# Performance work log

Hardware: AMD Instinct MI355X
Metric: run time of the kernel (lower is better)

## Reference

```python
import jax, jax.numpy as jnp
import numpy as np

B_SZ, SEQ, H, P, N, LBLK = 16, 2048, 16, 64, 16, 64  # batch, seqlen, heads, d_head, d_state, block_len


def setup_inputs() -> dict:
    key = jax.random.key(0)
    k1, k2, k3, k4 = jax.random.split(key, 4)
    X = jax.random.normal(k1, (B_SZ, SEQ, H, P), jnp.float32)
    # A is a per-step log-decay; real Mamba2 has A < 0 so exp(segsum) stays bounded
    A = -0.1 * jax.random.uniform(k2, (B_SZ, SEQ, H), jnp.float32)
    B = jax.random.normal(k3, (B_SZ, SEQ, H, N), jnp.float32)
    C = jax.random.normal(k4, (B_SZ, SEQ, H, N), jnp.float32)
    return {"X": X, "A": A, "B": B, "C": C}


def _exp_segsum(x):
    """x: (..., t). Returns exp(cumsum[i]-cumsum[j]) for j<=i, 0 above diagonal."""
    t = x.shape[-1]
    cs = jnp.cumsum(x, axis=-1)
    diff = cs[..., :, None] - cs[..., None, :]
    mask = jnp.tril(jnp.ones((t, t), dtype=bool))
    return jnp.where(mask, jnp.exp(jnp.where(mask, diff, 0.0)), 0.0)


def ssd_forward(X, A, B, C):
    b, s, h, p = X.shape
    n = B.shape[-1]
    c = s // LBLK
    # chunk: (b, c, l, h, *)
    Xb = X.reshape(b, c, LBLK, h, p)
    Bb = B.reshape(b, c, LBLK, h, n)
    Cb = C.reshape(b, c, LBLK, h, n)
    Ab = jnp.transpose(A.reshape(b, c, LBLK, h), (0, 3, 1, 2))  # (b, h, c, l)
    A_cs = jnp.cumsum(Ab, axis=-1)                               # (b, h, c, l)

    # 1. intra-chunk (diagonal block) output: kernel 1
    L = _exp_segsum(Ab)                                          # (b, h, c, l, s)
    CB = jnp.einsum("bclhn,bcshn->bhcls", Cb, Bb)               # (b, h, c, l, s)
    Y_diag = jnp.einsum("bhcls,bcshp->bclhp", CB * L, Xb)

    # 2. per-chunk end states: kernel 2
    decay_states = jnp.exp(A_cs[..., -1:] - A_cs)                # (b, h, c, l)
    states = jnp.einsum("bclhn,bhcl,bclhp->bchpn", Bb, decay_states, Xb)

    # 3. inter-chunk recurrence (zero initial state): kernel 3
    states = jnp.concatenate([jnp.zeros_like(states[:, :1]), states], axis=1)  # (b, c+1, h, p, n)
    A_last_pad = jnp.pad(A_cs[..., -1], ((0, 0), (0, 0), (1, 0)))              # (b, h, c+1)
    decay_chunk = _exp_segsum(A_last_pad)                                       # (b, h, c+1, c+1)
    new_states = jnp.einsum("bhzc,bchpn->bzhpn", decay_chunk, states)
    states_in = new_states[:, :-1]                                              # (b, c, h, p, n)

    # 4. off-diagonal (state -> output) contribution: kernel 4
    Y_off = jnp.einsum("bclhn,bchpn,bhcl->bclhp", Cb, states_in, jnp.exp(A_cs))

    return (Y_diag + Y_off).reshape(b, s, h, p)


def reference(X, A, B, C):
    return ssd_forward(X, A, B, C)
```

## Files before the change

kernel.cpp:

```cpp
#include <hip/hip_runtime.h>

#define BS 16
#define SEQL 2048
#define NH 16
#define PD 64
#define ND 16
#define LB 64
#define NC 32
#define NHP (NH * PD)
#define NHN (NH * ND)

typedef __attribute__((ext_vector_type(8))) short bf16x8;
typedef __attribute__((ext_vector_type(4))) float f32x4;

static __device__ __forceinline__ unsigned short f2bf(float x) {
  unsigned int u = __float_as_uint(x);
  return (unsigned short)((u + 0x7FFFu + ((u >> 16) & 1u)) >> 16);
}
static __device__ __forceinline__ unsigned int pk2(float a, float b) {
  return (unsigned int)f2bf(a) | ((unsigned int)f2bf(b) << 16);
}

static __device__ __forceinline__ void barrier_lds() {
  __builtin_amdgcn_sched_barrier(0);
  asm volatile("s_waitcnt lgkmcnt(0)" ::: "memory");
  __builtin_amdgcn_s_barrier();
  __builtin_amdgcn_sched_barrier(0);
}

__global__ __launch_bounds__(512, 2) void ssd_fused(
    const float* __restrict__ Xg, const float* __restrict__ Ag,
    const float* __restrict__ Bg, const float* __restrict__ Cg,
    float* __restrict__ Yg) {
  const int h = blockIdx.x & (NH - 1);
  const int b = blockIdx.x >> 4;
  const int t = threadIdx.x;
  const int w = t >> 6;
  const int lane = t & 63;
  const int g = lane >> 4;
  const int cc = lane & 15;

  __shared__ __align__(16) unsigned short sXt[PD][LB + 8];
  __shared__ __align__(16) unsigned short sM [LB][LB + 8];
  __shared__ __align__(16) unsigned short sB [LB][ND + 8];
  __shared__ __align__(16) unsigned short sC [LB][ND + 8];
  __shared__ __align__(16) unsigned short sBdT[ND][LB + 8];
  __shared__ __align__(16) float          sSTf[2][PD][ND + 4];
  __shared__ __align__(16) unsigned short sSTb[2][PD][ND + 8];

  for (int i = t; i < PD * (ND + 4); i += 512) ((float*)sSTf[0])[i] = 0.f;
  for (int i = t; i < PD * (ND + 8); i += 512) ((unsigned short*)sSTb[0])[i] = 0;

  const int xl0 = (t >> 4) * 2, xp0 = (t & 15) * 4;
  const int bl  = t >> 3,       bn0 = (t & 7) * 2;
  float4 px0, px1; float2 pb2, pc2; float pa;

#define PREF(cc_) do { \
    const size_t s0_ = (size_t)(b * SEQL + (cc_) * LB); \
    px0 = *(const float4*)&Xg[(s0_ + xl0) * NHP + h * PD + xp0]; \
    px1 = *(const float4*)&Xg[(s0_ + xl0 + 1) * NHP + h * PD + xp0]; \
    pb2 = *(const float2*)&Bg[(s0_ + bl) * NHN + h * ND + bn0]; \
    pc2 = *(const float2*)&Cg[(s0_ + bl) * NHN + h * ND + bn0]; \
    pa  = Ag[(s0_ + lane) * NH + h]; \
  } while (0)

  PREF(0);

  for (int c = 0; c < NC; ++c) {
    float v = pa;
#pragma unroll
    for (int d = 1; d < 64; d <<= 1) {
      float o = __shfl_up(v, d, 64);
      if (lane >= d) v += o;
    }
    const float acs = v;
    const float er = expf(acs);
    const float rr = expf(-acs);
    const float etot = __shfl(er, 63);

    {
#pragma unroll
      for (int j = 0; j < 4; ++j) {
        const float xa = (&px0.x)[j], xb = (&px1.x)[j];
        *(unsigned int*)&sXt[xp0 + j][xl0] = pk2(xa, xb);
      }
      const float el = __shfl(er, bl);
      const float dl = etot * __shfl(rr, bl);
      *(unsigned int*)&sB[bl][bn0] = pk2(pb2.x, pb2.y);
      *(unsigned int*)&sC[bl][bn0] = pk2(el * pc2.x, el * pc2.y);
      sBdT[bn0][bl]     = f2bf(dl * pb2.x);
      sBdT[bn0 + 1][bl] = f2bf(dl * pb2.y);
    }
    if (c + 1 < NC) PREF(c + 1);
    barrier_lds();

    {
      const int lb1 = w & 3;
      const int l = lb1 * 16 + cc;
      bf16x8 zf = {0, 0, 0, 0, 0, 0, 0, 0};
      bf16x8 cf = zf;
      if (g < 2) cf = *(const bf16x8*)&sC[l][g * 8];
#pragma unroll
      for (int ii = 0; ii < 2; ++ii) {
        const int sb = (w < 4 ? 0 : 2) + ii;
        uint2 out = make_uint2(0u, 0u);
        if (sb <= lb1) {
          bf16x8 bfr = zf;
          if (g < 2) bfr = *(const bf16x8*)&sB[sb * 16 + cc][g * 8];
          f32x4 z4 = {0.f, 0.f, 0.f, 0.f};
          f32x4 d = __builtin_amdgcn_mfma_f32_16x16x32_bf16(bfr, cf, z4, 0, 0, 0);
          float m[4];
#pragma unroll
          for (int r = 0; r < 4; ++r) {
            const int srow = sb * 16 + 4 * g + r;
            m[r] = d[r] * __shfl(rr, srow);
            if (sb == lb1 && (4 * g + r) > cc) m[r] = 0.f;
          }
          out.x = pk2(m[0], m[1]);
          out.y = pk2(m[2], m[3]);
        }
        *(uint2*)&sM[l][sb * 16 + g * 4] = out;
      }
    }
    barrier_lds();

    const int cur = c & 1, nxt = cur ^ 1;
    if (w < 4) {
      const int lb = w;
      const int l = lb * 16 + cc;
      bf16x8 zf = {0, 0, 0, 0, 0, 0, 0, 0};
      bf16x8 cf = zf;
      if (g < 2) cf = *(const bf16x8*)&sC[l][g * 8];
      bf16x8 a0 = *(const bf16x8*)&sM[l][g * 8];
      bf16x8 a1 = zf;
      if (lb >= 2) a1 = *(const bf16x8*)&sM[l][32 + g * 8];
#pragma unroll
      for (int pb = 0; pb < 4; ++pb) {
        const int p = pb * 16 + cc;
        bf16x8 stf = zf;
        if (g < 2) stf = *(const bf16x8*)&sSTb[cur][p][g * 8];
        f32x4 acc = {0.f, 0.f, 0.f, 0.f};
        acc = __builtin_amdgcn_mfma_f32_16x16x32_bf16(cf, stf, acc, 0, 0, 0);
        bf16x8 xf0 = *(const bf16x8*)&sXt[p][g * 8];
        acc = __builtin_amdgcn_mfma_f32_16x16x32_bf16(a0, xf0, acc, 0, 0, 0);
        if (lb >= 2) {
          bf16x8 xf1 = *(const bf16x8*)&sXt[p][32 + g * 8];
          acc = __builtin_amdgcn_mfma_f32_16x16x32_bf16(a1, xf1, acc, 0, 0, 0);
        }
        const size_t yb =
            ((size_t)(b * SEQL + c * LB + lb * 16 + 4 * g)) * NHP + h * PD + p;
#pragma unroll
        for (int r = 0; r < 4; ++r)
          Yg[yb + (size_t)r * NHP] = acc[r];
      }
    } else {
      const int pb = w - 4;
      const int p = pb * 16 + cc;
      bf16x8 ad0 = *(const bf16x8*)&sBdT[cc][g * 8];
      bf16x8 ad1 = *(const bf16x8*)&sBdT[cc][32 + g * 8];
      bf16x8 xt0 = *(const bf16x8*)&sXt[p][g * 8];
      bf16x8 xt1 = *(const bf16x8*)&sXt[p][32 + g * 8];
      f32x4 acc = {0.f, 0.f, 0.f, 0.f};
      acc = __builtin_amdgcn_mfma_f32_16x16x32_bf16(ad0, xt0, acc, 0, 0, 0);
      acc = __builtin_amdgcn_mfma_f32_16x16x32_bf16(ad1, xt1, acc, 0, 0, 0);
      float4 old = *(const float4*)&sSTf[cur][p][4 * g];
      float4 nw;
      nw.x = old.x * etot + acc[0];
      nw.y = old.y * etot + acc[1];
      nw.z = old.z * etot + acc[2];
      nw.w = old.w * etot + acc[3];
      *(float4*)&sSTf[nxt][p][4 * g] = nw;
      uint2 ub;
      ub.x = pk2(nw.x, nw.y);
      ub.y = pk2(nw.z, nw.w);
      *(uint2*)&sSTb[nxt][p][4 * g] = ub;
    }
    barrier_lds();
  }
#undef PREF
}

extern "C" void kernel_launch(void* const* d_in, const int* in_sizes, int n_in,
                              void* d_out, int out_size, void* d_ws, size_t ws_size,
                              hipStream_t stream) {
  (void)in_sizes; (void)n_in; (void)out_size; (void)d_ws; (void)ws_size;
  const float* X = (const float*)d_in[0];
  const float* A = (const float*)d_in[1];
  const float* B = (const float*)d_in[2];
  const float* C = (const float*)d_in[3];
  float* Y = (float*)d_out;
  ssd_fused<<<BS * NH, 512, 0, stream>>>(X, A, B, C, Y);
}
```

Before: 80.15 us.

## Keep decay matrix in registers, precompute cumsums, swizzle X tile in LDS

Precomputes all chunk cumsums and exponentials for A once into shared memory at kernel start, removing the per-chunk shuffle scan. Drops the sM LDS round-trip and one barrier per chunk by having each Y-wave compute its masked CB*L tiles directly into MFMA operand registers. It also XOR-swizzles the transposed X tile with a K-permutation so fragments load with fewer bank conflicts, and removes the occupancy hint from launch bounds. In exchange the Y waves take on the extra MFMA and scaling work, and the state waves sit idle during that phase.

```diff
diff --git a/kernel.cpp b/kernel.cpp
--- a/kernel.cpp
+++ b/kernel.cpp
@@ -28,7 +28,13 @@
   __builtin_amdgcn_sched_barrier(0);
 }
 
-__global__ __launch_bounds__(512, 2) void ssd_fused(
+static __device__ __forceinline__ int invperm(int l) {
+  const int jp = l >> 5, v = l & 31;
+  return jp * 32 + (v < 16 ? (((v >> 2) << 3) | (v & 3))
+                           : ((((v - 16) >> 2) << 3) | 4 | ((v - 16) & 3)));
+}
+
+__global__ __launch_bounds__(512) void ssd_fused(
     const float* __restrict__ Xg, const float* __restrict__ Ag,
     const float* __restrict__ Bg, const float* __restrict__ Cg,
     float* __restrict__ Yg) {
@@ -40,140 +46,155 @@
   const int g = lane >> 4;
   const int cc = lane & 15;
 
-  __shared__ __align__(16) unsigned short sXt[PD][LB + 8];
-  __shared__ __align__(16) unsigned short sM [LB][LB + 8];
-  __shared__ __align__(16) unsigned short sB [LB][ND + 8];
-  __shared__ __align__(16) unsigned short sC [LB][ND + 8];
+  __shared__ __align__(16) unsigned short sXt[PD][64];
+  __shared__ __align__(16) unsigned short sB[LB][ND + 8];
+  __shared__ __align__(16) unsigned short sC[LB][ND + 8];
   __shared__ __align__(16) unsigned short sBdT[ND][LB + 8];
-  __shared__ __align__(16) float          sSTf[2][PD][ND + 4];
+  __shared__ __align__(16) float sSTf[2][PD][ND + 4];
   __shared__ __align__(16) unsigned short sSTb[2][PD][ND + 8];
-
+  __shared__ float sER[NC][LB];
+  __shared__ float sRR[NC][LB];
+  __shared__ float sEtot[NC];
+
+  {
+    float av[4];
+#pragma unroll
+    for (int k = 0; k < 4; ++k)
+      av[k] = Ag[((size_t)(b * SEQL + (w + 8 * k) * LB + lane)) * NH + h];
+#pragma unroll
+    for (int k = 0; k < 4; ++k) {
+      const int c = w + 8 * k;
+      float v = av[k];
+#pragma unroll
+      for (int d = 1; d < 64; d <<= 1) {
+        float o = __shfl_up(v, d, 64);
+        if (lane >= d) v += o;
+      }
+      const float e = expf(v);
+      sER[c][lane] = e;
+      sRR[c][lane] = expf(-v);
+      if (lane == 63) sEtot[c] = e;
+    }
+  }
   for (int i = t; i < PD * (ND + 4); i += 512) ((float*)sSTf[0])[i] = 0.f;
   for (int i = t; i < PD * (ND + 8); i += 512) ((unsigned short*)sSTb[0])[i] = 0;
 
   const int xl0 = (t >> 4) * 2, xp0 = (t & 15) * 4;
-  const int bl  = t >> 3,       bn0 = (t & 7) * 2;
-  float4 px0, px1; float2 pb2, pc2; float pa;
-
-#define PREF(cc_) do { \
-    const size_t s0_ = (size_t)(b * SEQL + (cc_) * LB); \
+  const int bl = t >> 3, bn0 = (t & 7) * 2;
+  const int mX = invperm(xl0);
+  const int mB = invperm(bl);
+  float4 px0, px1;
+  float2 pb2, pc2;
+
+#define PREF(ci) do { \
+    const size_t s0_ = (size_t)(b * SEQL + (ci) * LB); \
     px0 = *(const float4*)&Xg[(s0_ + xl0) * NHP + h * PD + xp0]; \
     px1 = *(const float4*)&Xg[(s0_ + xl0 + 1) * NHP + h * PD + xp0]; \
     pb2 = *(const float2*)&Bg[(s0_ + bl) * NHN + h * ND + bn0]; \
     pc2 = *(const float2*)&Cg[(s0_ + bl) * NHN + h * ND + bn0]; \
-    pa  = Ag[(s0_ + lane) * NH + h]; \
   } while (0)
 
+  const bf16x8 zf8 = {0, 0, 0, 0, 0, 0, 0, 0};
+  auto xfrag = [&](int p_, int kb) -> bf16x8 {
+    return *(const bf16x8*)&sXt[p_][(kb ^ ((p_ >> 3) & 7)) << 3];
+  };
+
   PREF(0);
+  __syncthreads();
 
   for (int c = 0; c < NC; ++c) {
-    float v = pa;
-#pragma unroll
-    for (int d = 1; d < 64; d <<= 1) {
-      float o = __shfl_up(v, d, 64);
-      if (lane >= d) v += o;
-    }
-    const float acs = v;
-    const float er = expf(acs);
-    const float rr = expf(-acs);
-    const float etot = __shfl(er, 63);
-
     {
 #pragma unroll
       for (int j = 0; j < 4; ++j) {
-        const float xa = (&px0.x)[j], xb = (&px1.x)[j];
-        *(unsigned int*)&sXt[xp0 + j][xl0] = pk2(xa, xb);
-      }
-      const float el = __shfl(er, bl);
-      const float dl = etot * __shfl(rr, bl);
+        const int p_ = xp0 + j;
+        const int mm = ((((mX >> 3) ^ ((p_ >> 3) & 7)) << 3) | (mX & 7));
+        *(unsigned int*)&sXt[p_][mm] = pk2((&px0.x)[j], (&px1.x)[j]);
+      }
+      const float el = sER[c][bl];
+      const float dl = sEtot[c] * sRR[c][bl];
       *(unsigned int*)&sB[bl][bn0] = pk2(pb2.x, pb2.y);
       *(unsigned int*)&sC[bl][bn0] = pk2(el * pc2.x, el * pc2.y);
-      sBdT[bn0][bl]     = f2bf(dl * pb2.x);
-      sBdT[bn0 + 1][bl] = f2bf(dl * pb2.y);
+      sBdT[bn0][mB] = f2bf(dl * pb2.x);
+      sBdT[bn0 + 1][mB] = f2bf(dl * pb2.y);
     }
     if (c + 1 < NC) PREF(c + 1);
-    barrier_lds();
-
-    {
-      const int lb1 = w & 3;
-      const int l = lb1 * 16 + cc;
-      bf16x8 zf = {0, 0, 0, 0, 0, 0, 0, 0};
-      bf16x8 cf = zf;
-      if (g < 2) cf = *(const bf16x8*)&sC[l][g * 8];
-#pragma unroll
-      for (int ii = 0; ii < 2; ++ii) {
-        const int sb = (w < 4 ? 0 : 2) + ii;
-        uint2 out = make_uint2(0u, 0u);
-        if (sb <= lb1) {
-          bf16x8 bfr = zf;
-          if (g < 2) bfr = *(const bf16x8*)&sB[sb * 16 + cc][g * 8];
-          f32x4 z4 = {0.f, 0.f, 0.f, 0.f};
-          f32x4 d = __builtin_amdgcn_mfma_f32_16x16x32_bf16(bfr, cf, z4, 0, 0, 0);
-          float m[4];
-#pragma unroll
-          for (int r = 0; r < 4; ++r) {
-            const int srow = sb * 16 + 4 * g + r;
-            m[r] = d[r] * __shfl(rr, srow);
-            if (sb == lb1 && (4 * g + r) > cc) m[r] = 0.f;
-          }
-          out.x = pk2(m[0], m[1]);
-          out.y = pk2(m[2], m[3]);
-        }
-        *(uint2*)&sM[l][sb * 16 + g * 4] = out;
-      }
-    }
     barrier_lds();
 
     const int cur = c & 1, nxt = cur ^ 1;
     if (w < 4) {
       const int lb = w;
       const int l = lb * 16 + cc;
-      bf16x8 zf = {0, 0, 0, 0, 0, 0, 0, 0};
-      bf16x8 cf = zf;
+      bf16x8 cf = zf8;
       if (g < 2) cf = *(const bf16x8*)&sC[l][g * 8];
-      bf16x8 a0 = *(const bf16x8*)&sM[l][g * 8];
-      bf16x8 a1 = zf;
-      if (lb >= 2) a1 = *(const bf16x8*)&sM[l][32 + g * 8];
+      auto mtile = [&](int sb, bool mask) -> uint2 {
+        bf16x8 bfr = zf8;
+        if (g < 2) bfr = *(const bf16x8*)&sB[sb * 16 + cc][g * 8];
+        f32x4 z4 = {0.f, 0.f, 0.f, 0.f};
+        f32x4 d = __builtin_amdgcn_mfma_f32_16x16x32_bf16(bfr, cf, z4, 0, 0, 0);
+        float m[4];
+#pragma unroll
+        for (int r = 0; r < 4; ++r) {
+          m[r] = d[r] * sRR[c][sb * 16 + 4 * g + r];
+          if (mask && (4 * g + r) > cc) m[r] = 0.f;
+        }
+        return make_uint2(pk2(m[0], m[1]), pk2(m[2], m[3]));
+      };
+      union {
+        bf16x8 v;
+        unsigned int u[4];
+      } mf0, mf1;
+      mf0.u[0] = mf0.u[1] = mf0.u[2] = mf0.u[3] = 0u;
+      mf1.u[0] = mf1.u[1] = mf1.u[2] = mf1.u[3] = 0u;
+      if (lb == 0) {
+        const uint2 t0 = mtile(0, true);
+        mf0.u[0] = t0.x; mf0.u[1] = t0.y;
+      } else if (lb == 1) {
+        const uint2 t0 = mtile(0, false), t1 = mtile(1, true);
+        mf0.u[0] = t0.x; mf0.u[1] = t0.y; mf0.u[2] = t1.x; mf0.u[3] = t1.y;
+      } else if (lb == 2) {
+        const uint2 t0 = mtile(0, false), t1 = mtile(1, false), t2 = mtile(2, true);
+        mf0.u[0] = t0.x; mf0.u[1] = t0.y; mf0.u[2] = t1.x; mf0.u[3] = t1.y;
+        mf1.u[0] = t2.x; mf1.u[1] = t2.y;
+      } else {
+        const uint2 t0 = mtile(0, false), t1 = mtile(1, false);
+        const uint2 t2 = mtile(2, false), t3 = mtile(3, true);
+        mf0.u[0] = t0.x; mf0.u[1] = t0.y; mf0.u[2] = t1.x; mf0.u[3] = t1.y;
+        mf1.u[0] = t2.x; mf1.u[1] = t2.y; mf1.u[2] = t3.x; mf1.u[3] = t3.y;
+      }
 #pragma unroll
       for (int pb = 0; pb < 4; ++pb) {
         const int p = pb * 16 + cc;
-        bf16x8 stf = zf;
+        bf16x8 stf = zf8;
         if (g < 2) stf = *(const bf16x8*)&sSTb[cur][p][g * 8];
         f32x4 acc = {0.f, 0.f, 0.f, 0.f};
         acc = __builtin_amdgcn_mfma_f32_16x16x32_bf16(cf, stf, acc, 0, 0, 0);
-        bf16x8 xf0 = *(const bf16x8*)&sXt[p][g * 8];
-        acc = __builtin_amdgcn_mfma_f32_16x16x32_bf16(a0, xf0, acc, 0, 0, 0);
-        if (lb >= 2) {
-          bf16x8 xf1 = *(const bf16x8*)&sXt[p][32 + g * 8];
-          acc = __builtin_amdgcn_mfma_f32_16x16x32_bf16(a1, xf1, acc, 0, 0, 0);
-        }
+        acc = __builtin_amdgcn_mfma_f32_16x16x32_bf16(mf0.v, xfrag(p, g), acc, 0, 0, 0);
+        if (lb >= 2)
+          acc = __builtin_amdgcn_mfma_f32_16x16x32_bf16(mf1.v, xfrag(p, 4 + g), acc, 0, 0, 0);
         const size_t yb =
             ((size_t)(b * SEQL + c * LB + lb * 16 + 4 * g)) * NHP + h * PD + p;
 #pragma unroll
-        for (int r = 0; r < 4; ++r)
-          Yg[yb + (size_t)r * NHP] = acc[r];
+        for (int r = 0; r < 4; ++r) Yg[yb + (size_t)r * NHP] = acc[r];
       }
     } else {
-      const int pb = w - 4;
-      const int p = pb * 16 + cc;
+      const int pS = (w - 4) * 16 + cc;
       bf16x8 ad0 = *(const bf16x8*)&sBdT[cc][g * 8];
       bf16x8 ad1 = *(const bf16x8*)&sBdT[cc][32 + g * 8];
-      bf16x8 xt0 = *(const bf16x8*)&sXt[p][g * 8];
-      bf16x8 xt1 = *(const bf16x8*)&sXt[p][32 + g * 8];
-      f32x4 acc = {0.f, 0.f, 0.f, 0.f};
-      acc = __builtin_amdgcn_mfma_f32_16x16x32_bf16(ad0, xt0, acc, 0, 0, 0);
-      acc = __builtin_amdgcn_mfma_f32_16x16x32_bf16(ad1, xt1, acc, 0, 0, 0);
-      float4 old = *(const float4*)&sSTf[cur][p][4 * g];
+      f32x4 s4 = {0.f, 0.f, 0.f, 0.f};
+      s4 = __builtin_amdgcn_mfma_f32_16x16x32_bf16(ad0, xfrag(pS, g), s4, 0, 0, 0);
+      s4 = __builtin_amdgcn_mfma_f32_16x16x32_bf16(ad1, xfrag(pS, 4 + g), s4, 0, 0, 0);
+      const float etot = sEtot[c];
+      float4 old = *(const float4*)&sSTf[cur][pS][4 * g];
       float4 nw;
-      nw.x = old.x * etot + acc[0];
-      nw.y = old.y * etot + acc[1];
-      nw.z = old.z * etot + acc[2];
-      nw.w = old.w * etot + acc[3];
-      *(float4*)&sSTf[nxt][p][4 * g] = nw;
+      nw.x = old.x * etot + s4[0];
+      nw.y = old.y * etot + s4[1];
+      nw.z = old.z * etot + s4[2];
+      nw.w = old.w * etot + s4[3];
+      *(float4*)&sSTf[nxt][pS][4 * g] = nw;
       uint2 ub;
       ub.x = pk2(nw.x, nw.y);
       ub.y = pk2(nw.z, nw.w);
-      *(uint2*)&sSTb[nxt][p][4 * g] = ub;
+      *(uint2*)&sSTb[nxt][pS][4 * g] = ub;
     }
     barrier_lds();
   }
```

New measurement: 76.42 us. 4.7% less time.
